# Optimization experiments

Measured on AMD Instinct MI355X. Metric: run time of the kernel, lower is better.

Reference implementation:

```python
import jax, jax.numpy as jnp
import numpy as np

B, S, D, H = 1, 4096, 1024, 16
HD = D // H  # head_size = 64

def setup_inputs() -> dict:
    key = jax.random.key(0)
    ks = jax.random.split(key, 9)
    scale = 1.0 / np.sqrt(D)
    return {
        "x": jax.random.normal(ks[0], (B, S, D), jnp.float32),
        "Wq": jax.random.normal(ks[1], (D, D), jnp.float32) * scale,
        "bq": jax.random.normal(ks[2], (D,), jnp.float32) * 0.01,
        "Wk": jax.random.normal(ks[3], (D, D), jnp.float32) * scale,
        "bk": jax.random.normal(ks[4], (D,), jnp.float32) * 0.01,
        "Wv": jax.random.normal(ks[5], (D, D), jnp.float32) * scale,
        "bv": jax.random.normal(ks[6], (D,), jnp.float32) * 0.01,
        "Wo": jax.random.normal(ks[7], (D, D), jnp.float32) * scale,
        "bo": jax.random.normal(ks[8], (D,), jnp.float32) * 0.01,
    }

def _split_heads(t):
    # (B, S, D) -> (B, H, S, HD)
    return t.reshape(B, S, H, HD).transpose(0, 2, 1, 3)

def reference(x, Wq, bq, Wk, bk, Wv, bv, Wo, bo):
    q = _split_heads(x @ Wq + bq)
    k = _split_heads(x @ Wk + bk)
    v = _split_heads(x @ Wv + bv)
    # scores: (B, H, S, S), materialized as in the original naive attention
    scores = jnp.einsum('bhqd,bhkd->bhqk', q, k) / jnp.sqrt(jnp.asarray(HD, q.dtype))
    causal = jnp.tril(jnp.ones((S, S), dtype=bool))  # tril mask, broadcast over (B, H)
    scores = jnp.where(causal[None, None], scores, jnp.asarray(-1e9, scores.dtype))
    attn = jax.nn.softmax(scores, axis=-1)
    out = jnp.einsum('bhqk,bhkd->bhqd', attn, v)  # (B, H, S, HD)
    out = out.transpose(0, 2, 1, 3).reshape(B, S, D)  # combine heads
    return out @ Wo + bo
```

## Files before the change

### kernel.cpp

```cpp
#include <hip/hip_runtime.h>

#define SEQ 4096
#define DM  1024
#define NH  16
#define HDIM 64

typedef unsigned short u16;
typedef unsigned int   u32;
typedef __bf16 bf16x8 __attribute__((ext_vector_type(8)));
typedef float f32x4 __attribute__((ext_vector_type(4)));

__device__ __forceinline__ float bf2f(u16 u) {
    unsigned v = ((unsigned)u) << 16;
    float f;
    __builtin_memcpy(&f, &v, 4);
    return f;
}
__device__ __forceinline__ u16 f2bf(float f) {
    unsigned u;
    __builtin_memcpy(&u, &f, 4);
    return (u16)((u + 0x7fffu + ((u >> 16) & 1u)) >> 16);
}
__device__ __forceinline__ u32 bfpack(float a, float b) {
    u32 ua, ub;
    __builtin_memcpy(&ua, &a, 4);
    __builtin_memcpy(&ub, &b, 4);
    return ((ua + 0x8000u) >> 16) | ((ub + 0x8000u) & 0xffff0000u);
}

typedef const __attribute__((address_space(1))) unsigned int gas_uint;
typedef __attribute__((address_space(3))) unsigned int las_uint;
__device__ __forceinline__ void gld16(const u16* g, u16* l) {
    __builtin_amdgcn_global_load_lds((gas_uint*)g, (las_uint*)l, 16, 0, 0);
}

__device__ __forceinline__ f32x4 mfma16(bf16x8 a, bf16x8 b, f32x4 c) {
    return __builtin_amdgcn_mfma_f32_16x16x32_bf16(a, b, c, 0, 0, 0);
}

#define QSCALE 0.18033688011f

__global__ __launch_bounds__(256) void detect_k(const u16* __restrict__ w,
                                                int* __restrict__ flags) {
    __shared__ float red[256];
    const int t = threadIdx.x;
    float mx = 0.f;
    for (int i = t; i < 4096; i += 256) {
        float v = fabsf(bf2f(w[i]));
        if (v < 3e38f) mx = fmaxf(mx, v);
    }
    red[t] = mx;
    __syncthreads();
    for (int s = 128; s > 0; s >>= 1) {
        if (t < s) red[t] = fmaxf(red[t], red[t + s]);
        __syncthreads();
    }
    if (t == 0) {
        flags[0] = (red[0] > 1e4f) ? 1 : 0;
        flags[1] = 0;
    }
}

__global__ __launch_bounds__(256) void prep_w(const void* w0, const void* w1,
                                              const void* w2, const void* w3,
                                              const void* b0, const void* b1,
                                              const void* b2, const void* b3,
                                              u16* __restrict__ wt,
                                              u16* __restrict__ b_dst,
                                              const int* __restrict__ flags) {
    __shared__ u16 tile[32][33];
    const int f = flags[0];
    const int z = blockIdx.z;
    const void* win[4] = {w0, w1, w2, w3};
    const void* bin[4] = {b0, b1, b2, b3};
    const void* in = win[z];
    u16* out = wt + (size_t)z * DM * DM;
    const float scale = (z == 0) ? QSCALE : 1.0f;

    const int bx = blockIdx.x * 32;
    const int by = blockIdx.y * 32;
    const int tx = threadIdx.x & 31;
    const int ty = threadIdx.x >> 5;
#pragma unroll
    for (int i = ty; i < 32; i += 8) {
        size_t idx = (size_t)(by + i) * DM + bx + tx;
        float v = f ? ((const float*)in)[idx] : bf2f(((const u16*)in)[idx]);
        tile[i][tx] = f2bf(v * scale);
    }
    __syncthreads();
#pragma unroll
    for (int i = ty; i < 32; i += 8) out[(size_t)(bx + i) * DM + by + tx] = tile[tx][i];

    if (blockIdx.x == 0 && blockIdx.y == 0) {
        const void* bi = bin[z];
        for (int i = threadIdx.x; i < DM; i += 256) {
            float v = f ? ((const float*)bi)[i] : bf2f(((const u16*)bi)[i]);
            b_dst[z * DM + i] = f2bf(v * scale);
        }
    }
}

__global__ __launch_bounds__(256) void cvt_x8(const void* __restrict__ src,
                                              u16* __restrict__ dst,
                                              const int* __restrict__ flags) {
    const size_t i = ((size_t)blockIdx.x * 256 + threadIdx.x) * 8;
    if (flags[0]) {
        const float4* s4 = (const float4*)((const float*)src + i);
        float4 a = s4[0], b = s4[1];
        uint4 o;
        o.x = bfpack(a.x, a.y);
        o.y = bfpack(a.z, a.w);
        o.z = bfpack(b.x, b.y);
        o.w = bfpack(b.z, b.w);
        *(uint4*)(dst + i) = o;
    } else {
        *(uint4*)(dst + i) = *(const uint4*)((const u16*)src + i);
    }
}

__global__ __launch_bounds__(256, 2) void gemm128(const u16* __restrict__ A,
                                                  const u16* __restrict__ Bt,
                                                  const u16* __restrict__ bias,
                                                  void* __restrict__ C,
                                                  int M, int N, int K,
                                                  const int* __restrict__ flags) {
    __shared__ u16 As[128 * 32];
    __shared__ u16 Bs[128 * 32];
    const int f    = flags[0];
    const int tid  = threadIdx.x;
    const int lane = tid & 63;
    const int w    = tid >> 6;
    const int m    = lane & 15;
    const int quad = lane >> 4;
    const int wr   = w >> 1;
    const int wc   = w & 1;
    const int mb = blockIdx.x * 128;
    const int nb = blockIdx.y * 128;

    f32x4 acc[4][4] = {};

    for (int kb = 0; kb < K; kb += 32) {
        __syncthreads();
#pragma unroll
        for (int i = 0; i < 2; ++i) {
            const int Lb = i * 256 + w * 64;
            const int L  = Lb + lane;
            const int row = L >> 2, cb = L & 3;
            gld16(&A[(size_t)(mb + row) * K + kb + cb * 8], &As[Lb * 8]);
            gld16(&Bt[(size_t)(nb + row) * K + kb + cb * 8], &Bs[Lb * 8]);
        }
        __syncthreads();

        bf16x8 af[4];
#pragma unroll
        for (int mt = 0; mt < 4; ++mt)
            af[mt] = *(const bf16x8*)&As[(wr * 64 + mt * 16 + m) * 32 + quad * 8];
#pragma unroll
        for (int ct = 0; ct < 4; ++ct) {
            bf16x8 bfr = *(const bf16x8*)&Bs[(wc * 64 + ct * 16 + m) * 32 + quad * 8];
#pragma unroll
            for (int mt = 0; mt < 4; ++mt)
                acc[mt][ct] = mfma16(af[mt], bfr, acc[mt][ct]);
        }
    }

#pragma unroll
    for (int ct = 0; ct < 4; ++ct) {
        float bv = bf2f(bias[nb + wc * 64 + ct * 16 + m]);
#pragma unroll
        for (int mt = 0; mt < 4; ++mt) {
#pragma unroll
            for (int r = 0; r < 4; ++r) {
                int row = mb + wr * 64 + mt * 16 + quad * 4 + r;
                size_t idx = (size_t)row * N + nb + wc * 64 + ct * 16 + m;
                float v = acc[mt][ct][r] + bv;
                if (f) ((float*)C)[idx] = v;
                else   ((u16*)C)[idx]   = f2bf(v);
            }
        }
    }
}

__global__ __launch_bounds__(256) void vt_k(const u16* __restrict__ qkv,
                                            u16* __restrict__ Vt) {
    __shared__ u16 T[64][72];
    const int st = blockIdx.x;
    const int h  = blockIdx.y;
    const int t  = threadIdx.x;
    const int sl = t >> 2, c = t & 3;
    const u16* src = &qkv[(size_t)(st * 64 + sl) * 3072 + 2048 + h * 64 + c * 16];
    *(uint4*)&T[sl][c * 16]     = *(const uint4*)src;
    *(uint4*)&T[sl][c * 16 + 8] = *(const uint4*)(src + 8);
    __syncthreads();
    const int dl = t >> 2, c2 = t & 3;
    u16 tmp[16];
#pragma unroll
    for (int i = 0; i < 16; ++i) tmp[i] = T[c2 * 16 + i][dl];
    u16* dst = &Vt[(size_t)(h * 64 + dl) * SEQ + st * 64 + c2 * 16];
    *(uint4*)dst       = *(const uint4*)&tmp[0];
    *(uint4*)(dst + 8) = *(const uint4*)&tmp[8];
}

__global__ __launch_bounds__(256) void attn_split(const u16* __restrict__ QKV,
                                                  const u16* __restrict__ Vt,
                                                  u16* __restrict__ ab,
                                                  u16* __restrict__ slotB,
                                                  float* __restrict__ lA,
                                                  float* __restrict__ lB) {
    __shared__ u16 Ks[2][64 * 64];
    __shared__ u16 Vs[2][64 * 64];
    __shared__ u16 Ps[4][32 * 72];

    const int tid  = threadIdx.x;
    const int lane = tid & 63;
    const int w    = tid >> 6;
    const int m    = lane & 15;
    const int quad = lane >> 4;
    const int l3   = lane >> 3;
    const int cx   = ((lane & 7) ^ l3) * 8;
    const int xr8  = m & 7;

    const int b    = blockIdx.x;
    const int x    = b & 7;
    const int j    = b >> 3;
    const int h    = 2 * x + (j & 1);
    const int u    = j >> 1;
    const int qt   = 31 - (u >> 1);
    const int half = u & 1;
    const int k0t  = half ? qt + 1 : 0;
    const int k1t  = half ? 2 * qt + 1 : qt;
    const int hc   = h * HDIM;

    const int qbw = qt * 128 + w * 32;
    const int dkt = qbw >> 6;

    bf16x8 qf[2][2];
#pragma unroll
    for (int mt = 0; mt < 2; ++mt)
#pragma unroll
        for (int kh = 0; kh < 2; ++kh)
            qf[mt][kh] = *(const bf16x8*)&QKV[(size_t)(qbw + mt * 16 + m) * 3072 + hc + kh * 32 + quad * 8];

    f32x4 o_acc[2][4] = {};
    f32x4 l_part[2] = {};

#pragma unroll
    for (int i = 0; i < 2; ++i) {
        const int rsub = i * 8 + l3;
        gld16(&QKV[(size_t)(k0t * 64 + 4 * rsub + w) * 3072 + 1024 + hc + cx],
              &Ks[0][(w * 16 + i * 8) * 64]);
        gld16(&Vt[(size_t)(hc + w * 16 + rsub) * SEQ + k0t * 64 + cx],
              &Vs[0][(w * 16 + i * 8) * 64]);
    }

    for (int kt = k0t; kt <= k1t; ++kt) {
        const int cur = (kt - k0t) & 1;
        __syncthreads();

        if (kt < k1t) {
            const int nb = 1 - cur;
            const int nkt = kt + 1;
#pragma unroll
            for (int i = 0; i < 2; ++i) {
                const int rsub = i * 8 + l3;
                gld16(&QKV[(size_t)(nkt * 64 + 4 * rsub + w) * 3072 + 1024 + hc + cx],
                      &Ks[nb][(w * 16 + i * 8) * 64]);
                gld16(&Vt[(size_t)(hc + w * 16 + rsub) * SEQ + nkt * 64 + cx],
                      &Vs[nb][(w * 16 + i * 8) * 64]);
            }
        }

        if (kt > dkt) continue;

        const u16* ksb = Ks[cur];
        const u16* vsb = Vs[cur];

        f32x4 sc[2][4];
#pragma unroll
        for (int ct = 0; ct < 4; ++ct) {
            const int rb = (ct * 16 + m) * 64;
            bf16x8 k0 = *(const bf16x8*)&ksb[rb + ((quad ^ xr8) * 8)];
            bf16x8 k1 = *(const bf16x8*)&ksb[rb + (((quad + 4) ^ xr8) * 8)];
#pragma unroll
            for (int mt = 0; mt < 2; ++mt) {
                f32x4 a = {};
                a = mfma16(qf[mt][0], k0, a);
                a = mfma16(qf[mt][1], k1, a);
                sc[mt][ct] = a;
            }
        }

        if (kt < dkt) {
#pragma unroll
            for (int mt = 0; mt < 2; ++mt)
#pragma unroll
                for (int ct = 0; ct < 4; ++ct)
#pragma unroll
                    for (int r = 0; r < 4; ++r)
                        sc[mt][ct][r] = __builtin_amdgcn_exp2f(sc[mt][ct][r]);
        } else {
#pragma unroll
            for (int mt = 0; mt < 2; ++mt)
#pragma unroll
                for (int ct = 0; ct < 4; ++ct) {
                    const int jcol = kt * 64 + 4 * m + ct;
#pragma unroll
                    for (int r = 0; r < 4; ++r) {
                        const int i2 = qbw + mt * 16 + quad * 4 + r;
                        float p = __builtin_amdgcn_exp2f(sc[mt][ct][r]);
                        sc[mt][ct][r] = (jcol > i2) ? 0.f : p;
                    }
                }
        }

#pragma unroll
        for (int mt = 0; mt < 2; ++mt)
#pragma unroll
            for (int r = 0; r < 4; ++r)
                l_part[mt][r] += sc[mt][0][r] + sc[mt][1][r] + sc[mt][2][r] + sc[mt][3][r];

        u16* psw = (u16*)&Ps[w][0];
#pragma unroll
        for (int mt = 0; mt < 2; ++mt)
#pragma unroll
            for (int r = 0; r < 4; ++r) {
                uint2 val;
                val.x = bfpack(sc[mt][0][r], sc[mt][1][r]);
                val.y = bfpack(sc[mt][2][r], sc[mt][3][r]);
                *(uint2*)&psw[(mt * 16 + quad * 4 + r) * 72 + 4 * m] = val;
            }

        bf16x8 pf0[2], pf1[2];
#pragma unroll
        for (int mt = 0; mt < 2; ++mt) {
            pf0[mt] = *(const bf16x8*)&psw[(mt * 16 + m) * 72 + quad * 8];
            pf1[mt] = *(const bf16x8*)&psw[(mt * 16 + m) * 72 + 32 + quad * 8];
        }
#pragma unroll
        for (int ct = 0; ct < 4; ++ct) {
            const int rb = (ct * 16 + m) * 64;
            bf16x8 v0 = *(const bf16x8*)&vsb[rb + ((quad ^ xr8) * 8)];
            bf16x8 v1 = *(const bf16x8*)&vsb[rb + (((quad + 4) ^ xr8) * 8)];
#pragma unroll
            for (int mt = 0; mt < 2; ++mt) {
                o_acc[mt][ct] = mfma16(pf0[mt], v0, o_acc[mt][ct]);
                o_acc[mt][ct] = mfma16(pf1[mt], v1, o_acc[mt][ct]);
            }
        }
    }

#pragma unroll
    for (int off = 1; off < 16; off <<= 1)
#pragma unroll
        for (int mt = 0; mt < 2; ++mt)
#pragma unroll
            for (int r = 0; r < 4; ++r)
                l_part[mt][r] += __shfl_xor(l_part[mt][r], off, 64);

    u16*   dst = half ? slotB : ab;
    float* lb  = half ? lB : lA;
#pragma unroll
    for (int mt = 0; mt < 2; ++mt)
#pragma unroll
        for (int ct = 0; ct < 4; ++ct)
#pragma unroll
            for (int r = 0; r < 4; ++r) {
                int row = qbw + mt * 16 + quad * 4 + r;
                dst[(size_t)row * DM + hc + ct * 16 + m] = f2bf(o_acc[mt][ct][r]);
            }
    if (m == 0) {
#pragma unroll
        for (int mt = 0; mt < 2; ++mt)
#pragma unroll
            for (int r = 0; r < 4; ++r)
                lb[h * SEQ + qbw + mt * 16 + quad * 4 + r] = l_part[mt][r];
    }
}

__global__ __launch_bounds__(256) void merge_k(u16* __restrict__ ab,
                                               const u16* __restrict__ sB,
                                               const float* __restrict__ lA,
                                               const float* __restrict__ lB) {
    const int gid = blockIdx.x * 256 + threadIdx.x;
    const int rl = gid >> 7;
    const int cg = gid & 127;
    const int h  = cg >> 3;
    const float inv = 1.0f / (lA[h * SEQ + rl] + lB[h * SEQ + rl]);
    uint4 va = *(const uint4*)(ab + (size_t)rl * DM + cg * 8);
    uint4 vb = *(const uint4*)(sB + (size_t)rl * DM + cg * 8);
    const u16* a16 = (const u16*)&va;
    const u16* b16 = (const u16*)&vb;
    u16 oo[8];
#pragma unroll
    for (int i = 0; i < 8; ++i) oo[i] = f2bf((bf2f(a16[i]) + bf2f(b16[i])) * inv);
    *(uint4*)(ab + (size_t)rl * DM + cg * 8) = *(const uint4*)&oo[0];
}

extern "C" void kernel_launch(void* const* d_in, const int* in_sizes, int n_in,
                              void* d_out, int out_size, void* d_ws, size_t ws_size,
                              hipStream_t stream) {
    (void)in_sizes; (void)n_in; (void)out_size; (void)ws_size;

    u16* ws    = (u16*)d_ws;
    int* flags = (int*)d_ws;
    u16* xc    = ws + 64;
    u16* Vt_g  = xc;
    u16* Wtqkv = xc + (size_t)SEQ * DM;
    u16* Wto   = Wtqkv + (size_t)3 * DM * DM;
    u16* bqkv  = Wto + (size_t)DM * DM;
    u16* boc   = bqkv + 3 * DM;
    u16* qkv   = boc + DM;
    u16* ab    = qkv + (size_t)SEQ * 3 * DM;
    u16* slotB = ab + (size_t)SEQ * DM;
    float* lAf = (float*)Wtqkv;
    float* lBf = lAf + NH * SEQ;

    detect_k<<<1, 256, 0, stream>>>((const u16*)d_in[1], flags);

    prep_w<<<dim3(DM / 32, DM / 32, 4), 256, 0, stream>>>(
        d_in[1], d_in[3], d_in[5], d_in[7],
        d_in[2], d_in[4], d_in[6], d_in[8],
        Wtqkv, bqkv, flags);

    cvt_x8<<<SEQ * DM / 2048, 256, 0, stream>>>(d_in[0], xc, flags);

    gemm128<<<dim3(SEQ / 128, 3 * DM / 128), 256, 0, stream>>>(
        xc, Wtqkv, bqkv, qkv, SEQ, 3 * DM, DM, flags + 1);

    vt_k<<<dim3(SEQ / 64, NH), 256, 0, stream>>>(qkv, Vt_g);

    attn_split<<<dim3(1024), 256, 0, stream>>>(qkv, Vt_g, ab, slotB, lAf, lBf);

    merge_k<<<dim3(SEQ * 128 / 256), 256, 0, stream>>>(ab, slotB, lAf, lBf);

    gemm128<<<dim3(SEQ / 128, DM / 128), 256, 0, stream>>>(
        ab, Wto, boc, d_out, SEQ, DM, DM, flags);
}
```

Before: 230.1 us.

## Compute transposed S^T tiles to skip P LDS round-trip, 64-row waves

The attention kernel now computes S^T = K·Q^T with K as the A operand. The exponentiated scores then sit directly in the MFMA input layout, so P is fed to the PV MFMA from registers with zero padding in half the k-lanes, and the Ps shared-memory staging is removed. Each wave now owns 64 query rows instead of 32, giving 256 rows per block, and the grid is halved to 512 blocks with launch_bounds(256,2). This is meant to cut LDS traffic and raise K/V reuse per load. The cost is half-wasted MFMA k-lanes in the PV product, higher register pressure, and fewer blocks to balance the causal work.

```diff
diff --git a/kernel.cpp b/kernel.cpp
--- a/kernel.cpp
+++ b/kernel.cpp
@@ -201,15 +201,14 @@
     *(uint4*)(dst + 8) = *(const uint4*)&tmp[8];
 }
 
-__global__ __launch_bounds__(256) void attn_split(const u16* __restrict__ QKV,
-                                                  const u16* __restrict__ Vt,
-                                                  u16* __restrict__ ab,
-                                                  u16* __restrict__ slotB,
-                                                  float* __restrict__ lA,
-                                                  float* __restrict__ lB) {
+__global__ __launch_bounds__(256, 2) void attn_split(const u16* __restrict__ QKV,
+                                                     const u16* __restrict__ Vt,
+                                                     u16* __restrict__ ab,
+                                                     u16* __restrict__ slotB,
+                                                     float* __restrict__ lA,
+                                                     float* __restrict__ lB) {
     __shared__ u16 Ks[2][64 * 64];
     __shared__ u16 Vs[2][64 * 64];
-    __shared__ u16 Ps[4][32 * 72];
 
     const int tid  = threadIdx.x;
     const int lane = tid & 63;
@@ -218,39 +217,35 @@
     const int quad = lane >> 4;
     const int l3   = lane >> 3;
     const int cx   = ((lane & 7) ^ l3) * 8;
-    const int xr8  = m & 7;
-
-    const int b    = blockIdx.x;
-    const int x    = b & 7;
-    const int j    = b >> 3;
-    const int h    = 2 * x + (j & 1);
-    const int u    = j >> 1;
-    const int qt   = 31 - (u >> 1);
-    const int half = u & 1;
-    const int k0t  = half ? qt + 1 : 0;
-    const int k1t  = half ? 2 * qt + 1 : qt;
-    const int hc   = h * HDIM;
-
-    const int qbw = qt * 128 + w * 32;
-    const int dkt = qbw >> 6;
-
-    bf16x8 qf[2][2];
-#pragma unroll
-    for (int mt = 0; mt < 2; ++mt)
-#pragma unroll
-        for (int kh = 0; kh < 2; ++kh)
-            qf[mt][kh] = *(const bf16x8*)&QKV[(size_t)(qbw + mt * 16 + m) * 3072 + hc + kh * 32 + quad * 8];
-
-    f32x4 o_acc[2][4] = {};
-    f32x4 l_part[2] = {};
+    const int m7   = m & 7;
+
+    const int b = blockIdx.x;
+    const int x = b & 7;
+    const int u = b >> 3;
+    int qt2, head, half;
+    if (u < 32) { qt2 = 15 - (u >> 1); head = 2 * x + (u & 1);        half = 0; }
+    else        { int u2 = u - 32; qt2 = u2 >> 1; head = 2 * x + (u2 & 1); half = 1; }
+    const int hc  = head * HDIM;
+    const int k0t = half ? 2 * qt2 + 2 : 0;
+    const int k1t = half ? 4 * qt2 + 3 : 2 * qt2 + 1;
+    const int qw  = qt2 * 256 + w * 64;
+    const int dw  = qw >> 6;
+
+    bf16x8 qf[4][2];
+#pragma unroll
+    for (int qt4 = 0; qt4 < 4; ++qt4)
+#pragma unroll
+        for (int c = 0; c < 2; ++c)
+            qf[qt4][c] = *(const bf16x8*)&QKV[(size_t)(qw + qt4 * 16 + m) * 3072 + hc + c * 32 + quad * 8];
+
+    f32x4 o_acc[4][4] = {};
+    float l_part[4] = {0.f, 0.f, 0.f, 0.f};
 
 #pragma unroll
     for (int i = 0; i < 2; ++i) {
-        const int rsub = i * 8 + l3;
-        gld16(&QKV[(size_t)(k0t * 64 + 4 * rsub + w) * 3072 + 1024 + hc + cx],
-              &Ks[0][(w * 16 + i * 8) * 64]);
-        gld16(&Vt[(size_t)(hc + w * 16 + rsub) * SEQ + k0t * 64 + cx],
-              &Vs[0][(w * 16 + i * 8) * 64]);
+        const int r = w * 16 + i * 8 + l3;
+        gld16(&QKV[(size_t)(k0t * 64 + r) * 3072 + 1024 + hc + cx], &Ks[0][(w * 16 + i * 8) * 64]);
+        gld16(&Vt[(size_t)(hc + r) * SEQ + k0t * 64 + cx],           &Vs[0][(w * 16 + i * 8) * 64]);
     }
 
     for (int kt = k0t; kt <= k1t; ++kt) {
@@ -262,118 +257,99 @@
             const int nkt = kt + 1;
 #pragma unroll
             for (int i = 0; i < 2; ++i) {
-                const int rsub = i * 8 + l3;
-                gld16(&QKV[(size_t)(nkt * 64 + 4 * rsub + w) * 3072 + 1024 + hc + cx],
-                      &Ks[nb][(w * 16 + i * 8) * 64]);
-                gld16(&Vt[(size_t)(hc + w * 16 + rsub) * SEQ + nkt * 64 + cx],
-                      &Vs[nb][(w * 16 + i * 8) * 64]);
-            }
-        }
-
-        if (kt > dkt) continue;
+                const int r = w * 16 + i * 8 + l3;
+                gld16(&QKV[(size_t)(nkt * 64 + r) * 3072 + 1024 + hc + cx], &Ks[nb][(w * 16 + i * 8) * 64]);
+                gld16(&Vt[(size_t)(hc + r) * SEQ + nkt * 64 + cx],           &Vs[nb][(w * 16 + i * 8) * 64]);
+            }
+        }
+
+        if (kt > dw) continue;
 
         const u16* ksb = Ks[cur];
         const u16* vsb = Vs[cur];
 
-        f32x4 sc[2][4];
-#pragma unroll
-        for (int ct = 0; ct < 4; ++ct) {
-            const int rb = (ct * 16 + m) * 64;
-            bf16x8 k0 = *(const bf16x8*)&ksb[rb + ((quad ^ xr8) * 8)];
-            bf16x8 k1 = *(const bf16x8*)&ksb[rb + (((quad + 4) ^ xr8) * 8)];
-#pragma unroll
-            for (int mt = 0; mt < 2; ++mt) {
+#pragma unroll
+        for (int st = 0; st < 4; ++st) {
+            bf16x8 kf[2];
+#pragma unroll
+            for (int c = 0; c < 2; ++c)
+                kf[c] = *(const bf16x8*)&ksb[(st * 16 + m) * 64 + (((c * 4 + quad) ^ m7) * 8)];
+
+            f32x4 sc[4];
+#pragma unroll
+            for (int qt4 = 0; qt4 < 4; ++qt4) {
                 f32x4 a = {};
-                a = mfma16(qf[mt][0], k0, a);
-                a = mfma16(qf[mt][1], k1, a);
-                sc[mt][ct] = a;
-            }
-        }
-
-        if (kt < dkt) {
-#pragma unroll
-            for (int mt = 0; mt < 2; ++mt)
-#pragma unroll
-                for (int ct = 0; ct < 4; ++ct)
+                a = mfma16(kf[0], qf[qt4][0], a);
+                a = mfma16(kf[1], qf[qt4][1], a);
+                sc[qt4] = a;
+            }
+
+            if (kt == dw) {
+#pragma unroll
+                for (int qt4 = 0; qt4 < 4; ++qt4)
+#pragma unroll
+                    for (int r = 0; r < 4; ++r) {
+                        float p = __builtin_amdgcn_exp2f(sc[qt4][r]);
+                        sc[qt4][r] = (st * 16 + quad * 4 + r > qt4 * 16 + m) ? 0.f : p;
+                    }
+            } else {
+#pragma unroll
+                for (int qt4 = 0; qt4 < 4; ++qt4)
 #pragma unroll
                     for (int r = 0; r < 4; ++r)
-                        sc[mt][ct][r] = __builtin_amdgcn_exp2f(sc[mt][ct][r]);
-        } else {
-#pragma unroll
-            for (int mt = 0; mt < 2; ++mt)
-#pragma unroll
-                for (int ct = 0; ct < 4; ++ct) {
-                    const int jcol = kt * 64 + 4 * m + ct;
-#pragma unroll
-                    for (int r = 0; r < 4; ++r) {
-                        const int i2 = qbw + mt * 16 + quad * 4 + r;
-                        float p = __builtin_amdgcn_exp2f(sc[mt][ct][r]);
-                        sc[mt][ct][r] = (jcol > i2) ? 0.f : p;
-                    }
-                }
-        }
-
-#pragma unroll
-        for (int mt = 0; mt < 2; ++mt)
-#pragma unroll
-            for (int r = 0; r < 4; ++r)
-                l_part[mt][r] += sc[mt][0][r] + sc[mt][1][r] + sc[mt][2][r] + sc[mt][3][r];
-
-        u16* psw = (u16*)&Ps[w][0];
-#pragma unroll
-        for (int mt = 0; mt < 2; ++mt)
-#pragma unroll
-            for (int r = 0; r < 4; ++r) {
-                uint2 val;
-                val.x = bfpack(sc[mt][0][r], sc[mt][1][r]);
-                val.y = bfpack(sc[mt][2][r], sc[mt][3][r]);
-                *(uint2*)&psw[(mt * 16 + quad * 4 + r) * 72 + 4 * m] = val;
-            }
-
-        bf16x8 pf0[2], pf1[2];
-#pragma unroll
-        for (int mt = 0; mt < 2; ++mt) {
-            pf0[mt] = *(const bf16x8*)&psw[(mt * 16 + m) * 72 + quad * 8];
-            pf1[mt] = *(const bf16x8*)&psw[(mt * 16 + m) * 72 + 32 + quad * 8];
-        }
-#pragma unroll
-        for (int ct = 0; ct < 4; ++ct) {
-            const int rb = (ct * 16 + m) * 64;
-            bf16x8 v0 = *(const bf16x8*)&vsb[rb + ((quad ^ xr8) * 8)];
-            bf16x8 v1 = *(const bf16x8*)&vsb[rb + (((quad + 4) ^ xr8) * 8)];
-#pragma unroll
-            for (int mt = 0; mt < 2; ++mt) {
-                o_acc[mt][ct] = mfma16(pf0[mt], v0, o_acc[mt][ct]);
-                o_acc[mt][ct] = mfma16(pf1[mt], v1, o_acc[mt][ct]);
-            }
-        }
-    }
-
-#pragma unroll
-    for (int off = 1; off < 16; off <<= 1)
-#pragma unroll
-        for (int mt = 0; mt < 2; ++mt)
-#pragma unroll
-            for (int r = 0; r < 4; ++r)
-                l_part[mt][r] += __shfl_xor(l_part[mt][r], off, 64);
+                        sc[qt4][r] = __builtin_amdgcn_exp2f(sc[qt4][r]);
+            }
+
+#pragma unroll
+            for (int qt4 = 0; qt4 < 4; ++qt4)
+                l_part[qt4] += sc[qt4][0] + sc[qt4][1] + sc[qt4][2] + sc[qt4][3];
+
+            bf16x8 pa[4];
+#pragma unroll
+            for (int qt4 = 0; qt4 < 4; ++qt4) {
+                uint4 t;
+                t.x = bfpack(sc[qt4][0], sc[qt4][1]);
+                t.y = bfpack(sc[qt4][2], sc[qt4][3]);
+                t.z = 0; t.w = 0;
+                __builtin_memcpy(&pa[qt4], &t, 16);
+            }
+
+#pragma unroll
+            for (int dt = 0; dt < 4; ++dt) {
+                const int chx = ((2 * st + (quad >> 1)) ^ m7);
+                uint2 v2 = *(const uint2*)&vsb[(dt * 16 + m) * 64 + chx * 8 + (quad & 1) * 4];
+                uint4 t;
+                t.x = v2.x; t.y = v2.y; t.z = 0; t.w = 0;
+                bf16x8 vf;
+                __builtin_memcpy(&vf, &t, 16);
+#pragma unroll
+                for (int qt4 = 0; qt4 < 4; ++qt4)
+                    o_acc[qt4][dt] = mfma16(pa[qt4], vf, o_acc[qt4][dt]);
+            }
+        }
+    }
+
+#pragma unroll
+    for (int qt4 = 0; qt4 < 4; ++qt4) {
+        l_part[qt4] += __shfl_xor(l_part[qt4], 16, 64);
+        l_part[qt4] += __shfl_xor(l_part[qt4], 32, 64);
+    }
 
     u16*   dst = half ? slotB : ab;
     float* lb  = half ? lB : lA;
 #pragma unroll
-    for (int mt = 0; mt < 2; ++mt)
-#pragma unroll
-        for (int ct = 0; ct < 4; ++ct)
+    for (int qt4 = 0; qt4 < 4; ++qt4)
+#pragma unroll
+        for (int dt = 0; dt < 4; ++dt)
 #pragma unroll
             for (int r = 0; r < 4; ++r) {
-                int row = qbw + mt * 16 + quad * 4 + r;
-                dst[(size_t)row * DM + hc + ct * 16 + m] = f2bf(o_acc[mt][ct][r]);
-            }
-    if (m == 0) {
-#pragma unroll
-        for (int mt = 0; mt < 2; ++mt)
-#pragma unroll
-            for (int r = 0; r < 4; ++r)
-                lb[h * SEQ + qbw + mt * 16 + quad * 4 + r] = l_part[mt][r];
+                int row = qw + qt4 * 16 + quad * 4 + r;
+                dst[(size_t)row * DM + hc + dt * 16 + m] = f2bf(o_acc[qt4][dt][r]);
+            }
+    if (lane < 16) {
+#pragma unroll
+        for (int qt4 = 0; qt4 < 4; ++qt4)
+            lb[head * SEQ + qw + qt4 * 16 + lane] = l_part[qt4];
     }
 }
 
@@ -429,7 +405,7 @@
 
     vt_k<<<dim3(SEQ / 64, NH), 256, 0, stream>>>(qkv, Vt_g);
 
-    attn_split<<<dim3(1024), 256, 0, stream>>>(qkv, Vt_g, ab, slotB, lAf, lBf);
+    attn_split<<<dim3(512), 256, 0, stream>>>(qkv, Vt_g, ab, slotB, lAf, lBf);
 
     merge_k<<<dim3(SEQ * 128 / 256), 256, 0, stream>>>(ab, slotB, lAf, lBf);
 
```

Result: slower. 243.5 us (+5.8%).
